# Performance work log

Hardware: AMD Instinct MI355X
Metric: run time of the kernel (lower is better)

## Reference

```python
import jax, jax.numpy as jnp
import numpy as np

DIM = 1024
NUM_EXPERTS = 8
TOP_K = 2
LOAD_BALANCE_WEIGHT = 0.01


def setup_inputs() -> dict:
    key = jax.random.key(0)
    ks = jax.random.split(key, 8)
    d, e, h = DIM, NUM_EXPERTS, 4 * DIM
    scale = 0.02
    return {
        "x": jax.random.normal(ks[0], (4, 2048, d), dtype=jnp.float32),
        "w_router": jax.random.normal(ks[1], (d, e), dtype=jnp.float32) * scale,
        "b_router": jnp.zeros((e,), dtype=jnp.float32),
        "w1": jax.random.normal(ks[2], (e, d, h), dtype=jnp.float32) * scale,
        "b1": jnp.zeros((e, h), dtype=jnp.float32),
        "w2": jax.random.normal(ks[3], (e, h, d), dtype=jnp.float32) * scale,
        "b2": jnp.zeros((e, d), dtype=jnp.float32),
    }


def reference(x, w_router, b_router, w1, b1, w2, b2):
    # x: [b, s, d]
    router_logits = jnp.einsum("bsd,de->bse", x, w_router) + b_router  # [b,s,E]
    probs = jax.nn.softmax(router_logits, axis=-1)
    routing_weights, selected_experts = jax.lax.top_k(probs, TOP_K)  # [b,s,K]
    routing_weights = routing_weights / routing_weights.sum(axis=-1, keepdims=True)

    output = jnp.zeros_like(x)
    for e in range(NUM_EXPERTS):
        # Dense per-expert MLP; tokens not routed to expert e get gate 0,
        # matching the masked scatter-add in the original module.
        h = jax.nn.gelu(jnp.einsum("bsd,dh->bsh", x, w1[e]) + b1[e], approximate=False)
        y = jnp.einsum("bsh,hd->bsd", h, w2[e]) + b2[e]
        gate = jnp.where(selected_experts == e, routing_weights, 0.0).sum(axis=-1)  # [b,s]
        output = output + y * gate[..., None]

    # Load-balance aux loss: var (unbiased, ddof=1) / mean of tokens-per-expert.
    one_hot = jax.nn.one_hot(selected_experts, NUM_EXPERTS, dtype=jnp.float32)  # [b,s,K,E]
    tokens_per_expert = one_hot.sum(axis=(0, 1, 2))  # [E]
    load_balance_loss = (jnp.var(tokens_per_expert, ddof=1) / tokens_per_expert.mean()) * LOAD_BALANCE_WEIGHT
    return output, load_balance_loss
```

## Files before the change

kernel.cpp:

```cpp
#include <hip/hip_runtime.h>
#include <math.h>

#define TOKENS 8192
#define DIM    1024
#define NEXP   8
#define HID    4096
#define TILE_M 128
#define MAX_TILES 136
#define BKS    32

#define BK     32
#define LDA    40
#define LDB    40

typedef __bf16 bf16x8 __attribute__((ext_vector_type(8)));
typedef float  f32x4  __attribute__((ext_vector_type(4)));
typedef unsigned int u32x4 __attribute__((ext_vector_type(4)));

__device__ __forceinline__ unsigned short f2bf(float f) {
  union { float f; unsigned u; } v; v.f = f;
  unsigned u = v.u + 0x7fffu + ((v.u >> 16) & 1u);
  return (unsigned short)(u >> 16);
}
__device__ __forceinline__ float gelu_f(float v) {
  return 0.5f * v * (1.f + erff(v * 0.7071067811865476f));
}
__device__ __forceinline__ void gload16(const void* g, void* l) {
  __builtin_amdgcn_global_load_lds(
      (const __attribute__((address_space(1))) void*)g,
      (__attribute__((address_space(3))) void*)l, 16, 0, 0);
}

__global__ __launch_bounds__(256) void k_router(
    const float* __restrict__ x, const float* __restrict__ wr,
    const float* __restrict__ br, int* __restrict__ sel,
    float* __restrict__ gates, int* __restrict__ counts,
    unsigned short* __restrict__ xb)
{
  int t = blockIdx.x * 4 + (threadIdx.x >> 6);
  int lane = threadIdx.x & 63;
  const float* xr = x + (size_t)t * DIM;
  unsigned short* xo = xb + (size_t)t * DIM;
  float acc[NEXP];
#pragma unroll
  for (int e = 0; e < NEXP; ++e) acc[e] = 0.f;
#pragma unroll
  for (int it = 0; it < 4; ++it) {
    int d = it * 256 + lane * 4;
    float4 xv = *(const float4*)(xr + d);
    ushort4 pk;
    pk.x = f2bf(xv.x); pk.y = f2bf(xv.y); pk.z = f2bf(xv.z); pk.w = f2bf(xv.w);
    *(ushort4*)(xo + d) = pk;
    float xs[4] = {xv.x, xv.y, xv.z, xv.w};
#pragma unroll
    for (int j = 0; j < 4; ++j) {
      float4 wa = *(const float4*)(wr + (size_t)(d + j) * NEXP);
      float4 wb = *(const float4*)(wr + (size_t)(d + j) * NEXP + 4);
      acc[0] += xs[j] * wa.x; acc[1] += xs[j] * wa.y;
      acc[2] += xs[j] * wa.z; acc[3] += xs[j] * wa.w;
      acc[4] += xs[j] * wb.x; acc[5] += xs[j] * wb.y;
      acc[6] += xs[j] * wb.z; acc[7] += xs[j] * wb.w;
    }
  }
#pragma unroll
  for (int off = 32; off >= 1; off >>= 1) {
#pragma unroll
    for (int e = 0; e < NEXP; ++e) acc[e] += __shfl_xor(acc[e], off);
  }
  if (lane == 0) {
    float l[NEXP];
#pragma unroll
    for (int e = 0; e < NEXP; ++e) l[e] = acc[e] + br[e];
    int e1 = 0; float v1 = l[0];
#pragma unroll
    for (int e = 1; e < NEXP; ++e) if (l[e] > v1) { v1 = l[e]; e1 = e; }
    int e2 = -1; float v2 = -1e30f;
#pragma unroll
    for (int e = 0; e < NEXP; ++e) {
      if (e == e1) continue;
      if (l[e] > v2) { v2 = l[e]; e2 = e; }
    }
    float g1 = 1.f / (1.f + expf(v2 - v1));
    sel[t * 2] = e1; sel[t * 2 + 1] = e2;
    gates[t * 2] = g1; gates[t * 2 + 1] = 1.f - g1;
    atomicAdd(&counts[e1], 1);
    atomicAdd(&counts[e2], 1);
  }
}

__global__ void k_setup(const int* __restrict__ counts, int* __restrict__ cursors,
                        int* __restrict__ ntiles_p, int* __restrict__ tile_expert,
                        int* __restrict__ tile_row0, int* __restrict__ pair_token,
                        float* __restrict__ pair_gate, float* __restrict__ loss_out)
{
  if (threadIdx.x != 0) return;
  int poff = 0, nt = 0;
  float var = 0.f;
  for (int e = 0; e < NEXP; ++e) {
    int c = counts[e];
    cursors[e] = poff;
    int ntl = (c + TILE_M - 1) / TILE_M;
    for (int i = 0; i < ntl; ++i) { tile_expert[nt] = e; tile_row0[nt] = poff + i * TILE_M; ++nt; }
    for (int r = poff + c; r < poff + ntl * TILE_M; ++r) { pair_token[r] = -1; pair_gate[r] = 0.f; }
    float d = (float)c - 2048.f;
    var += d * d;
    poff += ntl * TILE_M;
  }
  *ntiles_p = nt;
  var *= (1.f / 7.f);
  *loss_out = var * (1.f / 2048.f) * 0.01f;
}

__global__ __launch_bounds__(256) void k_bucket(
    const int* __restrict__ sel, const float* __restrict__ gates,
    int* __restrict__ cursors, int* __restrict__ pair_token, float* __restrict__ pair_gate)
{
  int t = blockIdx.x * 256 + threadIdx.x;
#pragma unroll
  for (int k = 0; k < 2; ++k) {
    int e = sel[t * 2 + k];
    int pos = atomicAdd(&cursors[e], 1);
    pair_token[pos] = t;
    pair_gate[pos] = gates[t * 2 + k];
  }
}

__global__ __launch_bounds__(256) void k_castwT(
    const float* __restrict__ w, unsigned short* __restrict__ wT, int K, int N)
{
  __shared__ unsigned short t[64][72];
  int e = blockIdx.z, n0 = blockIdx.x * 64, k0 = blockIdx.y * 64;
  int tid = threadIdx.x;
  int kr = tid >> 2, nc = (tid & 3) * 16;
  const float* src = w + ((size_t)e * K + k0 + kr) * N + n0 + nc;
#pragma unroll
  for (int j = 0; j < 4; ++j) {
    f32x4 v = *(const f32x4*)(src + j * 4);
#pragma unroll
    for (int q = 0; q < 4; ++q) t[nc + j * 4 + q][kr] = f2bf(v[q]);
  }
  __syncthreads();
  int nr = tid >> 2, kc = (tid & 3) * 16;
  unsigned short* dst = wT + ((size_t)e * N + n0 + nr) * K + k0 + kc;
  *(u32x4*)dst = *(const u32x4*)&t[nr][kc];
  *(u32x4*)(dst + 8) = *(const u32x4*)&t[nr][kc + 8];
}

__global__ __launch_bounds__(256) void k_gemm1n(
    const unsigned short* __restrict__ xb, const unsigned short* __restrict__ w1T,
    const float* __restrict__ b1, const int* __restrict__ pair_token,
    const int* __restrict__ tile_expert, const int* __restrict__ tile_row0,
    const int* __restrict__ ntiles_p, unsigned short* __restrict__ h, int chunk_base)
{
  int tile = chunk_base + blockIdx.y;
  if (tile >= *ntiles_p) return;
  const int e = tile_expert[tile];
  const int row0 = tile_row0[tile];
  const int n0 = blockIdx.x * 128;
  const int tid = threadIdx.x;
  const int w = tid >> 6, lane = tid & 63;

  __shared__ unsigned short As[128 * BKS];
  __shared__ unsigned short Bs[128 * BKS];
  __shared__ int tok[128];

  if (tid < 128) { int t = pair_token[row0 + tid]; tok[tid] = (t < 0) ? 0 : t; }
  __syncthreads();

  const int sr = lane >> 2;
  const int kq = (lane & 3) * 8;
  const int ar1 = w * 32 + sr, ar2 = ar1 + 16;
  const unsigned short* ag1 = xb + (size_t)tok[ar1] * DIM + kq;
  const unsigned short* ag2 = xb + (size_t)tok[ar2] * DIM + kq;
  const unsigned short* bg1 = w1T + ((size_t)e * HID + n0 + ar1) * DIM + kq;
  const unsigned short* bg2 = w1T + ((size_t)e * HID + n0 + ar2) * DIM + kq;
  unsigned short* la1 = &As[(w * 32) * BKS];
  unsigned short* la2 = &As[(w * 32 + 16) * BKS];
  unsigned short* lb1 = &Bs[(w * 32) * BKS];
  unsigned short* lb2 = &Bs[(w * 32 + 16) * BKS];

  const int wm = (w & 1) * 64, wn = (w >> 1) * 64;
  const int lr = lane & 15, lk = lane >> 4;

  f32x4 acc[4][4];
#pragma unroll
  for (int mi = 0; mi < 4; ++mi)
#pragma unroll
    for (int ni = 0; ni < 4; ++ni) acc[mi][ni] = {0.f, 0.f, 0.f, 0.f};

  for (int k0 = 0; k0 < DIM; k0 += BKS) {
    gload16(ag1 + k0, la1);
    gload16(ag2 + k0, la2);
    gload16(bg1 + k0, lb1);
    gload16(bg2 + k0, lb2);
    __syncthreads();
    bf16x8 af[4], bfr[4];
#pragma unroll
    for (int mi = 0; mi < 4; ++mi)
      af[mi] = *(const bf16x8*)&As[(wm + mi * 16 + lr) * BKS + lk * 8];
#pragma unroll
    for (int ni = 0; ni < 4; ++ni)
      bfr[ni] = *(const bf16x8*)&Bs[(wn + ni * 16 + lr) * BKS + lk * 8];
#pragma unroll
    for (int mi = 0; mi < 4; ++mi)
#pragma unroll
      for (int ni = 0; ni < 4; ++ni)
        acc[mi][ni] = __builtin_amdgcn_mfma_f32_16x16x32_bf16(af[mi], bfr[ni], acc[mi][ni], 0, 0, 0);
    __syncthreads();
  }

  const size_t tl = (size_t)(tile - chunk_base);
  float bia[4];
#pragma unroll
  for (int ni = 0; ni < 4; ++ni) bia[ni] = b1[(size_t)e * HID + n0 + wn + ni * 16 + lr];
#pragma unroll
  for (int mi = 0; mi < 4; ++mi)
#pragma unroll
    for (int r = 0; r < 4; ++r) {
      int m = wm + mi * 16 + lk * 4 + r;
#pragma unroll
      for (int ni = 0; ni < 4; ++ni) {
        int n = wn + ni * 16 + lr;
        h[(tl * TILE_M + m) * HID + n0 + n] = f2bf(gelu_f(acc[mi][ni][r] + bia[ni]));
      }
    }
}

__global__ __launch_bounds__(256) void k_gemm2n(
    const unsigned short* __restrict__ h, const unsigned short* __restrict__ w2T,
    const float* __restrict__ b2, const int* __restrict__ pair_token,
    const float* __restrict__ pair_gate,
    const int* __restrict__ tile_expert, const int* __restrict__ tile_row0,
    const int* __restrict__ ntiles_p, float* __restrict__ out, int chunk_base)
{
  int tile = chunk_base + blockIdx.y;
  if (tile >= *ntiles_p) return;
  const int e = tile_expert[tile];
  const int row0 = tile_row0[tile];
  const int n0 = blockIdx.x * 128;
  const int tid = threadIdx.x;
  const int w = tid >> 6, lane = tid & 63;

  __shared__ unsigned short As[128 * BKS];
  __shared__ unsigned short Bs[128 * BKS];
  __shared__ int tok[128];
  __shared__ float gat[128];

  if (tid < 128) { tok[tid] = pair_token[row0 + tid]; gat[tid] = pair_gate[row0 + tid]; }
  __syncthreads();

  const int sr = lane >> 2;
  const int kq = (lane & 3) * 8;
  const int ar1 = w * 32 + sr, ar2 = ar1 + 16;
  const size_t tl = (size_t)(tile - chunk_base);
  const unsigned short* ag1 = h + (tl * TILE_M + ar1) * HID + kq;
  const unsigned short* ag2 = h + (tl * TILE_M + ar2) * HID + kq;
  const unsigned short* bg1 = w2T + ((size_t)e * DIM + n0 + ar1) * HID + kq;
  const unsigned short* bg2 = w2T + ((size_t)e * DIM + n0 + ar2) * HID + kq;
  unsigned short* la1 = &As[(w * 32) * BKS];
  unsigned short* la2 = &As[(w * 32 + 16) * BKS];
  unsigned short* lb1 = &Bs[(w * 32) * BKS];
  unsigned short* lb2 = &Bs[(w * 32 + 16) * BKS];

  const int wm = (w & 1) * 64, wn = (w >> 1) * 64;
  const int lr = lane & 15, lk = lane >> 4;

  f32x4 acc[4][4];
#pragma unroll
  for (int mi = 0; mi < 4; ++mi)
#pragma unroll
    for (int ni = 0; ni < 4; ++ni) acc[mi][ni] = {0.f, 0.f, 0.f, 0.f};

  for (int k0 = 0; k0 < HID; k0 += BKS) {
    gload16(ag1 + k0, la1);
    gload16(ag2 + k0, la2);
    gload16(bg1 + k0, lb1);
    gload16(bg2 + k0, lb2);
    __syncthreads();
    bf16x8 af[4], bfr[4];
#pragma unroll
    for (int mi = 0; mi < 4; ++mi)
      af[mi] = *(const bf16x8*)&As[(wm + mi * 16 + lr) * BKS + lk * 8];
#pragma unroll
    for (int ni = 0; ni < 4; ++ni)
      bfr[ni] = *(const bf16x8*)&Bs[(wn + ni * 16 + lr) * BKS + lk * 8];
#pragma unroll
    for (int mi = 0; mi < 4; ++mi)
#pragma unroll
      for (int ni = 0; ni < 4; ++ni)
        acc[mi][ni] = __builtin_amdgcn_mfma_f32_16x16x32_bf16(af[mi], bfr[ni], acc[mi][ni], 0, 0, 0);
    __syncthreads();
  }

  float bia[4];
#pragma unroll
  for (int ni = 0; ni < 4; ++ni) bia[ni] = b2[(size_t)e * DIM + n0 + wn + ni * 16 + lr];
#pragma unroll
  for (int mi = 0; mi < 4; ++mi)
#pragma unroll
    for (int r = 0; r < 4; ++r) {
      int m = wm + mi * 16 + lk * 4 + r;
      int t = tok[m];
      if (t >= 0) {
        float g = gat[m];
#pragma unroll
        for (int ni = 0; ni < 4; ++ni) {
          int n = wn + ni * 16 + lr;
          atomicAdd(out + (size_t)t * DIM + n0 + n, (acc[mi][ni][r] + bia[ni]) * g);
        }
      }
    }
}

__global__ __launch_bounds__(256) void k_gemm1(
    const unsigned short* __restrict__ xb, const float* __restrict__ w1,
    const float* __restrict__ b1, const int* __restrict__ pair_token,
    const int* __restrict__ tile_expert, const int* __restrict__ tile_row0,
    const int* __restrict__ ntiles_p, unsigned short* __restrict__ h, int chunk_base)
{
  int tile = chunk_base + blockIdx.y;
  if (tile >= *ntiles_p) return;
  const int e = tile_expert[tile];
  const int row0 = tile_row0[tile];
  const int n0 = blockIdx.x * 128;
  const int tid = threadIdx.x;

  __shared__ unsigned short As[TILE_M * LDA];
  __shared__ unsigned short Bs[128 * LDB];
  __shared__ int tok[TILE_M];

  if (tid < TILE_M) tok[tid] = pair_token[row0 + tid];
  __syncthreads();

  const int ar = tid >> 1, akh = (tid & 1) * 16;
  const int bk = tid >> 3, bnh = (tid & 7) * 16;
  const int bswz = tid & 3;
  const int wv = tid >> 6, lane = tid & 63;
  const int wm = (wv & 1) * 64, wn = (wv >> 1) * 64;
  const int lr = lane & 15, lk = lane >> 4;
  const int atok = tok[ar];

  f32x4 acc[4][4];
#pragma unroll
  for (int mi = 0; mi < 4; ++mi)
#pragma unroll
    for (int ni = 0; ni < 4; ++ni) acc[mi][ni] = {0.f, 0.f, 0.f, 0.f};

  const unsigned short* asrc = (atok >= 0) ? (xb + (size_t)atok * DIM + akh) : (const unsigned short*)0;
  const float* bsrc0 = w1 + ((size_t)e * DIM + bk) * HID + n0 + bnh;
  const int wcol = 8 * ((bk >> 3) ^ bswz) + (bk & 7);

  for (int k0 = 0; k0 < DIM; k0 += BK) {
    u32x4 av0 = {0, 0, 0, 0}, av1 = {0, 0, 0, 0};
    if (asrc) {
      av0 = *(const u32x4*)(asrc + k0);
      av1 = *(const u32x4*)(asrc + k0 + 8);
    }
    float bv[16];
    const float* bs = bsrc0 + (size_t)k0 * HID;
#pragma unroll
    for (int j = 0; j < 4; ++j) {
      f32x4 f = *(const f32x4*)(bs + j * 4);
      bv[j * 4 + 0] = f[0]; bv[j * 4 + 1] = f[1];
      bv[j * 4 + 2] = f[2]; bv[j * 4 + 3] = f[3];
    }
    __syncthreads();
    *(u32x4*)&As[ar * LDA + akh] = av0;
    *(u32x4*)&As[ar * LDA + akh + 8] = av1;
#pragma unroll
    for (int j = 0; j < 16; ++j)
      Bs[(bnh + j) * LDB + wcol] = f2bf(bv[j]);
    __syncthreads();

    bf16x8 af[4], bfr[4];
#pragma unroll
    for (int mi = 0; mi < 4; ++mi)
      af[mi] = *(const bf16x8*)&As[(wm + mi * 16 + lr) * LDA + lk * 8];
#pragma unroll
    for (int ni = 0; ni < 4; ++ni) {
      int pch = lk ^ (((wn >> 4) + ni) & 3);
      bfr[ni] = *(const bf16x8*)&Bs[(wn + ni * 16 + lr) * LDB + pch * 8];
    }
#pragma unroll
    for (int mi = 0; mi < 4; ++mi)
#pragma unroll
      for (int ni = 0; ni < 4; ++ni)
        acc[mi][ni] = __builtin_amdgcn_mfma_f32_16x16x32_bf16(af[mi], bfr[ni], acc[mi][ni], 0, 0, 0);
  }

  const size_t tl = (size_t)(tile - chunk_base);
#pragma unroll
  for (int mi = 0; mi < 4; ++mi)
#pragma unroll
    for (int ni = 0; ni < 4; ++ni)
#pragma unroll
      for (int r = 0; r < 4; ++r) {
        int m = wm + mi * 16 + (lane >> 4) * 4 + r;
        int n = wn + ni * 16 + (lane & 15);
        float v = acc[mi][ni][r] + b1[(size_t)e * HID + n0 + n];
        h[(tl * TILE_M + m) * HID + n0 + n] = f2bf(gelu_f(v));
      }
}

__global__ __launch_bounds__(256) void k_gemm2(
    const unsigned short* __restrict__ h, const float* __restrict__ w2,
    const float* __restrict__ b2, const int* __restrict__ pair_token,
    const float* __restrict__ pair_gate,
    const int* __restrict__ tile_expert, const int* __restrict__ tile_row0,
    const int* __restrict__ ntiles_p, float* __restrict__ out, int chunk_base)
{
  int tile = chunk_base + blockIdx.y;
  if (tile >= *ntiles_p) return;
  const int e = tile_expert[tile];
  const int row0 = tile_row0[tile];
  const int n0 = blockIdx.x * 128;
  const int tid = threadIdx.x;

  __shared__ unsigned short As[TILE_M * LDA];
  __shared__ unsigned short Bs[128 * LDB];
  __shared__ int tok[TILE_M];
  __shared__ float gat[TILE_M];

  if (tid < TILE_M) { tok[tid] = pair_token[row0 + tid]; gat[tid] = pair_gate[row0 + tid]; }
  __syncthreads();

  const int ar = tid >> 1, akh = (tid & 1) * 16;
  const int bk = tid >> 3, bnh = (tid & 7) * 16;
  const int bswz = tid & 3;
  const int wv = tid >> 6, lane = tid & 63;
  const int wm = (wv & 1) * 64, wn = (wv >> 1) * 64;
  const int lr = lane & 15, lk = lane >> 4;

  f32x4 acc[4][4];
#pragma unroll
  for (int mi = 0; mi < 4; ++mi)
#pragma unroll
    for (int ni = 0; ni < 4; ++ni) acc[mi][ni] = {0.f, 0.f, 0.f, 0.f};

  const size_t tl = (size_t)(tile - chunk_base);
  const unsigned short* asrc = h + (tl * TILE_M + ar) * HID + akh;
  const float* bsrc0 = w2 + ((size_t)e * HID + bk) * DIM + n0 + bnh;
  const int wcol = 8 * ((bk >> 3) ^ bswz) + (bk & 7);

  for (int k0 = 0; k0 < HID; k0 += BK) {
    u32x4 av0 = *(const u32x4*)(asrc + k0);
    u32x4 av1 = *(const u32x4*)(asrc + k0 + 8);
    float bv[16];
    const float* bs = bsrc0 + (size_t)k0 * DIM;
#pragma unroll
    for (int j = 0; j < 4; ++j) {
      f32x4 f = *(const f32x4*)(bs + j * 4);
      bv[j * 4 + 0] = f[0]; bv[j * 4 + 1] = f[1];
      bv[j * 4 + 2] = f[2]; bv[j * 4 + 3] = f[3];
    }
    __syncthreads();
    *(u32x4*)&As[ar * LDA + akh] = av0;
    *(u32x4*)&As[ar * LDA + akh + 8] = av1;
#pragma unroll
    for (int j = 0; j < 16; ++j)
      Bs[(bnh + j) * LDB + wcol] = f2bf(bv[j]);
    __syncthreads();

    bf16x8 af[4], bfr[4];
#pragma unroll
    for (int mi = 0; mi < 4; ++mi)
      af[mi] = *(const bf16x8*)&As[(wm + mi * 16 + lr) * LDA + lk * 8];
#pragma unroll
    for (int ni = 0; ni < 4; ++ni) {
      int pch = lk ^ (((wn >> 4) + ni) & 3);
      bfr[ni] = *(const bf16x8*)&Bs[(wn + ni * 16 + lr) * LDB + pch * 8];
    }
#pragma unroll
    for (int mi = 0; mi < 4; ++mi)
#pragma unroll
      for (int ni = 0; ni < 4; ++ni)
        acc[mi][ni] = __builtin_amdgcn_mfma_f32_16x16x32_bf16(af[mi], bfr[ni], acc[mi][ni], 0, 0, 0);
  }

#pragma unroll
  for (int mi = 0; mi < 4; ++mi)
#pragma unroll
    for (int ni = 0; ni < 4; ++ni)
#pragma unroll
      for (int r = 0; r < 4; ++r) {
        int m = wm + mi * 16 + (lane >> 4) * 4 + r;
        int n = wn + ni * 16 + (lane & 15);
        int t = tok[m];
        if (t >= 0) {
          float v = acc[mi][ni][r] + b2[(size_t)e * DIM + n0 + n];
          atomicAdd(out + (size_t)t * DIM + n0 + n, v * gat[m]);
        }
      }
}

extern "C" void kernel_launch(void* const* d_in, const int* in_sizes, int n_in,
                              void* d_out, int out_size, void* d_ws, size_t ws_size,
                              hipStream_t stream) {
  const float* x  = (const float*)d_in[0];
  const float* wr = (const float*)d_in[1];
  const float* br = (const float*)d_in[2];
  const float* w1 = (const float*)d_in[3];
  const float* b1 = (const float*)d_in[4];
  const float* w2 = (const float*)d_in[5];
  const float* b2 = (const float*)d_in[6];
  float* out = (float*)d_out;

  char* ws = (char*)d_ws;
  int*   counts      = (int*)(ws + 0);
  int*   cursors     = (int*)(ws + 64);
  int*   ntiles      = (int*)(ws + 128);
  int*   tile_expert = (int*)(ws + 256);
  int*   tile_row0   = (int*)(ws + 1024);
  int*   sel         = (int*)(ws + 4096);
  float* gates       = (float*)(ws + 4096 + 65536);
  int*   pair_token  = (int*)(ws + 4096 + 131072);
  float* pair_gate   = (float*)(ws + 4096 + 131072 + 69632);

  const size_t OFF_XB  = 274432;
  const size_t XB_SZ   = (size_t)TOKENS * DIM * 2;
  const size_t OFF_W1T = OFF_XB + XB_SZ;
  const size_t WT_SZ   = (size_t)NEXP * DIM * HID * 2;
  const size_t OFF_W2T = OFF_W1T + WT_SZ;
  const size_t OFF_HN  = OFF_W2T + WT_SZ;
  const size_t tile_bytes = (size_t)TILE_M * HID * 2;

  unsigned short* xb  = (unsigned short*)(ws + OFF_XB);

  hipMemsetAsync(d_out, 0, (size_t)out_size * sizeof(float), stream);
  hipMemsetAsync(counts, 0, 64, stream);

  hipLaunchKernelGGL(k_router, dim3(TOKENS / 4), dim3(256), 0, stream,
                     x, wr, br, sel, gates, counts, xb);
  hipLaunchKernelGGL(k_setup, dim3(1), dim3(64), 0, stream,
                     counts, cursors, ntiles, tile_expert, tile_row0,
                     pair_token, pair_gate, out + (size_t)out_size - 1);
  hipLaunchKernelGGL(k_bucket, dim3(TOKENS / 256), dim3(256), 0, stream,
                     sel, gates, cursors, pair_token, pair_gate);

  bool newpath = ws_size >= OFF_HN + tile_bytes;

  if (newpath) {
    unsigned short* w1T = (unsigned short*)(ws + OFF_W1T);
    unsigned short* w2T = (unsigned short*)(ws + OFF_W2T);
    unsigned short* h   = (unsigned short*)(ws + OFF_HN);

    hipLaunchKernelGGL(k_castwT, dim3(HID / 64, DIM / 64, NEXP), dim3(256), 0, stream,
                       w1, w1T, DIM, HID);
    hipLaunchKernelGGL(k_castwT, dim3(DIM / 64, HID / 64, NEXP), dim3(256), 0, stream,
                       w2, w2T, HID, DIM);

    long long avail = (long long)ws_size - (long long)OFF_HN;
    int tpc = (int)(avail / (long long)tile_bytes);
    if (tpc < 1) tpc = 1;
    if (tpc > MAX_TILES) tpc = MAX_TILES;
    int nchunks = (MAX_TILES + tpc - 1) / tpc;

    for (int c = 0; c < nchunks; ++c) {
      hipLaunchKernelGGL(k_gemm1n, dim3(HID / 128, tpc), dim3(256), 0, stream,
                         xb, w1T, b1, pair_token, tile_expert, tile_row0, ntiles, h, c * tpc);
      hipLaunchKernelGGL(k_gemm2n, dim3(DIM / 128, tpc), dim3(256), 0, stream,
                         h, w2T, b2, pair_token, pair_gate, tile_expert, tile_row0, ntiles, out, c * tpc);
    }
  } else {
    unsigned short* h = (unsigned short*)(ws + OFF_W1T);
    long long avail = (long long)ws_size - (long long)OFF_W1T;
    int tpc = (avail > 0) ? (int)(avail / (long long)tile_bytes) : 0;
    if (tpc < 1) tpc = 1;
    if (tpc > MAX_TILES) tpc = MAX_TILES;
    int nchunks = (MAX_TILES + tpc - 1) / tpc;

    for (int c = 0; c < nchunks; ++c) {
      hipLaunchKernelGGL(k_gemm1, dim3(HID / 128, tpc), dim3(256), 0, stream,
                         xb, w1, b1, pair_token, tile_expert, tile_row0, ntiles, h, c * tpc);
      hipLaunchKernelGGL(k_gemm2, dim3(DIM / 128, tpc), dim3(256), 0, stream,
                         h, w2, b2, pair_token, pair_gate, tile_expert, tile_row0, ntiles, out, c * tpc);
    }
  }
}
```

Measured before the change: 864.5 us.

## Double-buffer LDS in expert GEMMs and swizzle workgroups across XCDs

```diff
diff --git a/kernel.cpp b/kernel.cpp
--- a/kernel.cpp
+++ b/kernel.cpp
@@ -29,6 +29,11 @@
   __builtin_amdgcn_global_load_lds(
       (const __attribute__((address_space(1))) void*)g,
       (__attribute__((address_space(3))) void*)l, 16, 0, 0);
+}
+__device__ __forceinline__ int xcd_swz(int id, int nwg) {
+  int q = nwg >> 3, r = nwg & 7;
+  int xcd = id & 7, rank = id >> 3;
+  return (xcd < r) ? xcd * (q + 1) + rank : r * (q + 1) + (xcd - r) * q + rank;
 }
 
 __global__ __launch_bounds__(256) void k_router(
@@ -152,16 +157,20 @@
     const int* __restrict__ tile_expert, const int* __restrict__ tile_row0,
     const int* __restrict__ ntiles_p, unsigned short* __restrict__ h, int chunk_base)
 {
-  int tile = chunk_base + blockIdx.y;
+  const int NBn = HID / 128;
+  const int nwg = gridDim.x;
+  int newid = xcd_swz(blockIdx.x, nwg);
+  int ltile = newid / NBn, nb = newid - ltile * NBn;
+  int tile = chunk_base + ltile;
   if (tile >= *ntiles_p) return;
   const int e = tile_expert[tile];
   const int row0 = tile_row0[tile];
-  const int n0 = blockIdx.x * 128;
+  const int n0 = nb * 128;
   const int tid = threadIdx.x;
   const int w = tid >> 6, lane = tid & 63;
 
-  __shared__ unsigned short As[128 * BKS];
-  __shared__ unsigned short Bs[128 * BKS];
+  __shared__ unsigned short As[2][128 * BKS];
+  __shared__ unsigned short Bs[2][128 * BKS];
   __shared__ int tok[128];
 
   if (tid < 128) { int t = pair_token[row0 + tid]; tok[tid] = (t < 0) ? 0 : t; }
@@ -174,10 +183,6 @@
   const unsigned short* ag2 = xb + (size_t)tok[ar2] * DIM + kq;
   const unsigned short* bg1 = w1T + ((size_t)e * HID + n0 + ar1) * DIM + kq;
   const unsigned short* bg2 = w1T + ((size_t)e * HID + n0 + ar2) * DIM + kq;
-  unsigned short* la1 = &As[(w * 32) * BKS];
-  unsigned short* la2 = &As[(w * 32 + 16) * BKS];
-  unsigned short* lb1 = &Bs[(w * 32) * BKS];
-  unsigned short* lb2 = &Bs[(w * 32 + 16) * BKS];
 
   const int wm = (w & 1) * 64, wn = (w >> 1) * 64;
   const int lr = lane & 15, lk = lane >> 4;
@@ -188,25 +193,48 @@
 #pragma unroll
     for (int ni = 0; ni < 4; ++ni) acc[mi][ni] = {0.f, 0.f, 0.f, 0.f};
 
-  for (int k0 = 0; k0 < DIM; k0 += BKS) {
-    gload16(ag1 + k0, la1);
-    gload16(ag2 + k0, la2);
-    gload16(bg1 + k0, lb1);
-    gload16(bg2 + k0, lb2);
-    __syncthreads();
+  {
+    unsigned short* la1 = &As[0][(w * 32) * BKS];
+    unsigned short* la2 = &As[0][(w * 32 + 16) * BKS];
+    unsigned short* lb1 = &Bs[0][(w * 32) * BKS];
+    unsigned short* lb2 = &Bs[0][(w * 32 + 16) * BKS];
+    gload16(ag1, la1); gload16(ag2, la2);
+    gload16(bg1, lb1); gload16(bg2, lb2);
+  }
+  asm volatile("s_waitcnt vmcnt(0)" ::: "memory");
+  __builtin_amdgcn_s_barrier();
+
+  const int NT = DIM / BKS;
+  int cur = 0;
+#pragma unroll 2
+  for (int t = 0; t < NT; ++t) {
+    int nxt = cur ^ 1;
+    if (t + 1 < NT) {
+      int k1 = (t + 1) * BKS;
+      gload16(ag1 + k1, &As[nxt][(w * 32) * BKS]);
+      gload16(ag2 + k1, &As[nxt][(w * 32 + 16) * BKS]);
+      gload16(bg1 + k1, &Bs[nxt][(w * 32) * BKS]);
+      gload16(bg2 + k1, &Bs[nxt][(w * 32 + 16) * BKS]);
+    }
     bf16x8 af[4], bfr[4];
 #pragma unroll
     for (int mi = 0; mi < 4; ++mi)
-      af[mi] = *(const bf16x8*)&As[(wm + mi * 16 + lr) * BKS + lk * 8];
+      af[mi] = *(const bf16x8*)&As[cur][(wm + mi * 16 + lr) * BKS + lk * 8];
 #pragma unroll
     for (int ni = 0; ni < 4; ++ni)
-      bfr[ni] = *(const bf16x8*)&Bs[(wn + ni * 16 + lr) * BKS + lk * 8];
+      bfr[ni] = *(const bf16x8*)&Bs[cur][(wn + ni * 16 + lr) * BKS + lk * 8];
+    asm volatile("s_waitcnt lgkmcnt(0)" ::: "memory");
+    __builtin_amdgcn_sched_barrier(0);
+    __builtin_amdgcn_s_setprio(1);
 #pragma unroll
     for (int mi = 0; mi < 4; ++mi)
 #pragma unroll
       for (int ni = 0; ni < 4; ++ni)
         acc[mi][ni] = __builtin_amdgcn_mfma_f32_16x16x32_bf16(af[mi], bfr[ni], acc[mi][ni], 0, 0, 0);
-    __syncthreads();
+    __builtin_amdgcn_s_setprio(0);
+    asm volatile("s_waitcnt vmcnt(0)" ::: "memory");
+    __builtin_amdgcn_s_barrier();
+    cur = nxt;
   }
 
   const size_t tl = (size_t)(tile - chunk_base);
@@ -233,16 +261,20 @@
     const int* __restrict__ tile_expert, const int* __restrict__ tile_row0,
     const int* __restrict__ ntiles_p, float* __restrict__ out, int chunk_base)
 {
-  int tile = chunk_base + blockIdx.y;
+  const int NBn = DIM / 128;
+  const int nwg = gridDim.x;
+  int newid = xcd_swz(blockIdx.x, nwg);
+  int ltile = newid / NBn, nb = newid - ltile * NBn;
+  int tile = chunk_base + ltile;
   if (tile >= *ntiles_p) return;
   const int e = tile_expert[tile];
   const int row0 = tile_row0[tile];
-  const int n0 = blockIdx.x * 128;
+  const int n0 = nb * 128;
   const int tid = threadIdx.x;
   const int w = tid >> 6, lane = tid & 63;
 
-  __shared__ unsigned short As[128 * BKS];
-  __shared__ unsigned short Bs[128 * BKS];
+  __shared__ unsigned short As[2][128 * BKS];
+  __shared__ unsigned short Bs[2][128 * BKS];
   __shared__ int tok[128];
   __shared__ float gat[128];
 
@@ -257,10 +289,6 @@
   const unsigned short* ag2 = h + (tl * TILE_M + ar2) * HID + kq;
   const unsigned short* bg1 = w2T + ((size_t)e * DIM + n0 + ar1) * HID + kq;
   const unsigned short* bg2 = w2T + ((size_t)e * DIM + n0 + ar2) * HID + kq;
-  unsigned short* la1 = &As[(w * 32) * BKS];
-  unsigned short* la2 = &As[(w * 32 + 16) * BKS];
-  unsigned short* lb1 = &Bs[(w * 32) * BKS];
-  unsigned short* lb2 = &Bs[(w * 32 + 16) * BKS];
 
   const int wm = (w & 1) * 64, wn = (w >> 1) * 64;
   const int lr = lane & 15, lk = lane >> 4;
@@ -271,25 +299,46 @@
 #pragma unroll
     for (int ni = 0; ni < 4; ++ni) acc[mi][ni] = {0.f, 0.f, 0.f, 0.f};
 
-  for (int k0 = 0; k0 < HID; k0 += BKS) {
-    gload16(ag1 + k0, la1);
-    gload16(ag2 + k0, la2);
-    gload16(bg1 + k0, lb1);
-    gload16(bg2 + k0, lb2);
-    __syncthreads();
+  {
+    gload16(ag1, &As[0][(w * 32) * BKS]);
+    gload16(ag2, &As[0][(w * 32 + 16) * BKS]);
+    gload16(bg1, &Bs[0][(w * 32) * BKS]);
+    gload16(bg2, &Bs[0][(w * 32 + 16) * BKS]);
+  }
+  asm volatile("s_waitcnt vmcnt(0)" ::: "memory");
+  __builtin_amdgcn_s_barrier();
+
+  const int NT = HID / BKS;
+  int cur = 0;
+#pragma unroll 2
+  for (int t = 0; t < NT; ++t) {
+    int nxt = cur ^ 1;
+    if (t + 1 < NT) {
+      int k1 = (t + 1) * BKS;
+      gload16(ag1 + k1, &As[nxt][(w * 32) * BKS]);
+      gload16(ag2 + k1, &As[nxt][(w * 32 + 16) * BKS]);
+      gload16(bg1 + k1, &Bs[nxt][(w * 32) * BKS]);
+      gload16(bg2 + k1, &Bs[nxt][(w * 32 + 16) * BKS]);
+    }
     bf16x8 af[4], bfr[4];
 #pragma unroll
     for (int mi = 0; mi < 4; ++mi)
-      af[mi] = *(const bf16x8*)&As[(wm + mi * 16 + lr) * BKS + lk * 8];
+      af[mi] = *(const bf16x8*)&As[cur][(wm + mi * 16 + lr) * BKS + lk * 8];
 #pragma unroll
     for (int ni = 0; ni < 4; ++ni)
-      bfr[ni] = *(const bf16x8*)&Bs[(wn + ni * 16 + lr) * BKS + lk * 8];
+      bfr[ni] = *(const bf16x8*)&Bs[cur][(wn + ni * 16 + lr) * BKS + lk * 8];
+    asm volatile("s_waitcnt lgkmcnt(0)" ::: "memory");
+    __builtin_amdgcn_sched_barrier(0);
+    __builtin_amdgcn_s_setprio(1);
 #pragma unroll
     for (int mi = 0; mi < 4; ++mi)
 #pragma unroll
       for (int ni = 0; ni < 4; ++ni)
         acc[mi][ni] = __builtin_amdgcn_mfma_f32_16x16x32_bf16(af[mi], bfr[ni], acc[mi][ni], 0, 0, 0);
-    __syncthreads();
+    __builtin_amdgcn_s_setprio(0);
+    asm volatile("s_waitcnt vmcnt(0)" ::: "memory");
+    __builtin_amdgcn_s_barrier();
+    cur = nxt;
   }
 
   float bia[4];
@@ -556,9 +605,9 @@
     int nchunks = (MAX_TILES + tpc - 1) / tpc;
 
     for (int c = 0; c < nchunks; ++c) {
-      hipLaunchKernelGGL(k_gemm1n, dim3(HID / 128, tpc), dim3(256), 0, stream,
+      hipLaunchKernelGGL(k_gemm1n, dim3(tpc * (HID / 128)), dim3(256), 0, stream,
                          xb, w1T, b1, pair_token, tile_expert, tile_row0, ntiles, h, c * tpc);
-      hipLaunchKernelGGL(k_gemm2n, dim3(DIM / 128, tpc), dim3(256), 0, stream,
+      hipLaunchKernelGGL(k_gemm2n, dim3(tpc * (DIM / 128)), dim3(256), 0, stream,
                          h, w2T, b2, pair_token, pair_gate, tile_expert, tile_row0, ntiles, out, c * tpc);
     }
   } else {
```

New measurement: 843.9 us. 1.02x faster.
